# Kernel tuning notes

Measured on AMD Instinct MI355X. Metric: run time of the kernel, lower is better.

## Reference

```python
import jax, jax.numpy as jnp
import numpy as np

B, N, DH = 256, 32, 128      # batch, n_agents, per-agent hidden
E = 496                       # n_edges (fully connected over 32 agents)
DIM_IN = 2 * DH               # 256, MLP input (concat of two agent states)
DIM_HID = 256
A = 12                        # dim_act
R = 4                         # payoff_rank
DIM_OUT = 2 * R * A           # 96


def setup_inputs() -> dict:
    key = jax.random.key(0)
    ks = jax.random.split(key, 7)
    hidden_states_n = jax.random.normal(ks[0], (B, N, DH), dtype=jnp.float32)
    edges_from = jax.random.randint(ks[1], (E,), 0, N, dtype=jnp.int32).astype(jnp.int64)
    edges_to = jax.random.randint(ks[2], (E,), 0, N, dtype=jnp.int32).astype(jnp.int64)
    # torch.nn.Linear params: W [out, in], b [out]
    W1 = jax.random.normal(ks[3], (DIM_HID, DIM_IN), dtype=jnp.float32) * (1.0 / np.sqrt(DIM_IN))
    b1 = jnp.zeros((DIM_HID,), dtype=jnp.float32)
    W2 = jax.random.normal(ks[4], (DIM_OUT, DIM_HID), dtype=jnp.float32) * (1.0 / np.sqrt(DIM_HID))
    b2 = jnp.zeros((DIM_OUT,), dtype=jnp.float32)
    return {"hidden_states_n": hidden_states_n, "W1": W1, "b1": b1, "W2": W2,
            "b2": b2, "edges_from": edges_from, "edges_to": edges_to}


def reference(hidden_states_n, W1, b1, W2, b2, edges_from, edges_to):
    hf = hidden_states_n[:, edges_from]                     # [B, E, DH]
    ht = hidden_states_n[:, edges_to]                       # [B, E, DH]
    # stack of (from||to, to||from): [2, B, E, 2*DH]
    inp = jnp.stack([jnp.concatenate([hf, ht], axis=-1),
                     jnp.concatenate([ht, hf], axis=-1)], axis=0)
    h = jax.nn.relu(inp @ W1.T + b1)                        # [2, B, E, DIM_HID]
    p = h @ W2.T + b2                                       # [2, B, E, 2*R*A]
    p = p.reshape(2, B, E, R, 2, A)
    # low-rank outer product per rank, summed over ranks: [2, B, E, A, A]
    payoffs = jnp.einsum('sberi,sberj->sbeij', p[..., 0, :], p[..., 1, :])
    # second copy is transposed, then mean over the two directions
    return 0.5 * (payoffs[0] + jnp.swapaxes(payoffs[1], -1, -2))  # [B, E, A, A]
```

## Files before the change

### kernel.cpp

```cpp
#include <hip/hip_runtime.h>

typedef unsigned int uint;
typedef unsigned short ushort_t;

typedef __attribute__((ext_vector_type(8))) short bf16x8;
typedef __attribute__((ext_vector_type(4))) float f32x4;

#define E_CNT 496

__device__ __forceinline__ ushort_t f32_to_bf16_rn(float x) {
    uint u = __float_as_uint(x);
    u = (u + 0x7fffu + ((u >> 16) & 1u)) >> 16;
    return (ushort_t)u;
}
__device__ __forceinline__ uint pack2_bf16(float lo, float hi) {
    return (uint)f32_to_bf16_rn(lo) | ((uint)f32_to_bf16_rn(hi) << 16);
}

__global__ __launch_bounds__(256) void prep_kernel(
    const int* __restrict__ sf, const int* __restrict__ st,
    const float* __restrict__ W1, const float* __restrict__ W2,
    int* __restrict__ ef, int* __restrict__ et,
    ushort_t* __restrict__ w1img, ushort_t* __restrict__ w2img) {
    const int tid = threadIdx.x;
    const int blk = blockIdx.x;
    if (blk < 32) {
        int gid = blk * 256 + tid;
        int half = gid >> 12;
        int rem = gid & 4095;
        int h = rem >> 4;
        int c = rem & 15;
        const float* src = W1 + h * 256 + half * 128 + c * 8;
        float4 v0 = *(const float4*)src;
        float4 v1 = *(const float4*)(src + 4);
        uint4 o;
        o.x = pack2_bf16(v0.x, v0.y);
        o.y = pack2_bf16(v0.z, v0.w);
        o.z = pack2_bf16(v1.x, v1.y);
        o.w = pack2_bf16(v1.z, v1.w);
        int dst = half * 32768 + h * 128 + ((c ^ (h & 7)) << 3);
        *(uint4*)(w1img + dst) = o;
    } else if (blk < 44) {
        int gid = (blk - 32) * 256 + tid;
        int n = gid >> 5;
        int c = gid & 31;
        const float* src = W2 + n * 256 + c * 8;
        float4 v0 = *(const float4*)src;
        float4 v1 = *(const float4*)(src + 4);
        uint4 o;
        o.x = pack2_bf16(v0.x, v0.y);
        o.y = pack2_bf16(v0.z, v0.w);
        o.z = pack2_bf16(v1.x, v1.y);
        o.w = pack2_bf16(v1.z, v1.w);
        *(uint4*)(w2img + n * 264 + c * 8) = o;
    } else {
        bool f64 = true, t64 = true;
        #pragma unroll
        for (int i = 0; i < 16; ++i) {
            if (sf[2 * i + 1] != 0) f64 = false;
            if (st[2 * i + 1] != 0) t64 = false;
        }
        for (int j = tid; j < E_CNT; j += 256) {
            ef[j] = f64 ? sf[2 * j] : sf[j];
            et[j] = t64 ? st[2 * j] : st[j];
        }
    }
}

__global__ __launch_bounds__(256) void x_kernel(
    const float* __restrict__ hidden, const ushort_t* __restrict__ w1img,
    const float* __restrict__ b1, ushort_t* __restrict__ Xout) {
    __shared__ __align__(16) ushort_t w1s[256 * 128];

    const int tid = threadIdx.x;
    const int half = blockIdx.x & 1;
    const int mblk = blockIdx.x >> 1;

    {
        const uint4* gsrc = (const uint4*)(w1img + half * 32768);
        uint4* ldst = (uint4*)w1s;
        #pragma unroll
        for (int j = 0; j < 16; ++j) ldst[tid + j * 256] = gsrc[tid + j * 256];
    }

    const int ln = tid & 63;
    const int waveId = tid >> 6;
    const int quad = ln >> 4;
    const int l16 = ln & 15;
    const int row0 = mblk * 64 + waveId * 16;

    union { uint u[4]; bf16x8 v; } af[4];
    const float* arow = hidden + (row0 + l16) * 128 + quad * 8;
    #pragma unroll
    for (int kk = 0; kk < 4; ++kk) {
        float4 v0 = *(const float4*)(arow + kk * 32);
        float4 v1 = *(const float4*)(arow + kk * 32 + 4);
        af[kk].u[0] = pack2_bf16(v0.x, v0.y);
        af[kk].u[1] = pack2_bf16(v0.z, v0.w);
        af[kk].u[2] = pack2_bf16(v1.x, v1.y);
        af[kk].u[3] = pack2_bf16(v1.z, v1.w);
    }
    __syncthreads();

    ushort_t* xbase = Xout + half * (8192 * 256);
    #pragma unroll
    for (int nt = 0; nt < 16; ++nt) {
        const int h = nt * 16 + l16;
        f32x4 acc = (f32x4){0.f, 0.f, 0.f, 0.f};
        #pragma unroll
        for (int kk = 0; kk < 4; ++kk) {
            const int c_log = kk * 4 + quad;
            bf16x8 bf = *(const bf16x8*)&w1s[h * 128 + ((c_log ^ (h & 7)) << 3)];
            acc = __builtin_amdgcn_mfma_f32_16x16x32_bf16(af[kk].v, bf, acc, 0, 0, 0);
        }
        const float bh = 0.5f * b1[h];
        #pragma unroll
        for (int r = 0; r < 4; ++r) {
            const int row = row0 + quad * 4 + r;
            xbase[row * 256 + h] = f32_to_bf16_rn(acc[r] + bh);
        }
    }
}

#define PAIR_STRIDE 100
#define R_OFF 800
#define WAVE_PF 1600

__global__ __launch_bounds__(512, 4) void gemm_payoff_kernel(
    const ushort_t* __restrict__ X1, const ushort_t* __restrict__ X2,
    const int* __restrict__ ef, const int* __restrict__ et,
    const ushort_t* __restrict__ w2img, const float* __restrict__ b2,
    float* __restrict__ out) {

    __shared__ __align__(16) unsigned char smem[51200];
    ushort_t* w2s = (ushort_t*)smem;
    float* pf = (float*)smem;

    const int tid = threadIdx.x;

    {
        const uint4* src = (const uint4*)w2img;
        uint4* dst = (uint4*)smem;
        #pragma unroll
        for (int j = 0; j < 7; ++j) {
            int idx = tid + j * 512;
            if (idx < 3168) dst[idx] = src[idx];
        }
    }

    const int ln = tid & 63;
    const int waveId = tid >> 6;
    const int quad = ln >> 4;
    const int l16 = ln & 15;
    const int pl = l16 & 7;
    const int s = l16 >> 3;

    const int pairBase = blockIdx.x * 128 + waveId * 16;
    const ushort_t* px1[2];
    const ushort_t* px2[2];
    #pragma unroll
    for (int mt = 0; mt < 2; ++mt) {
        int pair = pairBase + mt * 8 + pl;
        int b = pair / E_CNT;
        int e = pair - b * E_CNT;
        int f = ef[e];
        int t = et[e];
        int n1 = s ? t : f;
        int n2 = s ? f : t;
        px1[mt] = X1 + ((b * 32 + n1) * 256 + quad * 8);
        px2[mt] = X2 + ((b * 32 + n2) * 256 + quad * 8);
    }

    float b2v[6];
    #pragma unroll
    for (int tt = 0; tt < 6; ++tt) b2v[tt] = b2[tt * 16 + l16];

    f32x4 acc[2][6];
    #pragma unroll
    for (int mt = 0; mt < 2; ++mt)
        #pragma unroll
        for (int tt = 0; tt < 6; ++tt) acc[mt][tt] = (f32x4){0.f, 0.f, 0.f, 0.f};

    __syncthreads();

    #pragma unroll
    for (int kk = 0; kk < 8; ++kk) {
        union { uint u[4]; bf16x8 v; } af[2];
        #pragma unroll
        for (int mt = 0; mt < 2; ++mt) {
            uint4 a1 = *(const uint4*)(px1[mt] + kk * 32);
            uint4 a2 = *(const uint4*)(px2[mt] + kk * 32);
            uint ua[4] = {a1.x, a1.y, a1.z, a1.w};
            uint ub[4] = {a2.x, a2.y, a2.z, a2.w};
            #pragma unroll
            for (int w = 0; w < 4; ++w) {
                float lo = __uint_as_float(ua[w] << 16) + __uint_as_float(ub[w] << 16);
                float hi = __uint_as_float(ua[w] & 0xffff0000u) + __uint_as_float(ub[w] & 0xffff0000u);
                lo = fmaxf(lo, 0.f);
                hi = fmaxf(hi, 0.f);
                af[mt].u[w] = (__float_as_uint(lo) >> 16) | (__float_as_uint(hi) & 0xffff0000u);
            }
        }
        #pragma unroll
        for (int tt = 0; tt < 6; ++tt) {
            bf16x8 bf = *(const bf16x8*)&w2s[(tt * 16 + l16) * 264 + kk * 32 + quad * 8];
            acc[0][tt] = __builtin_amdgcn_mfma_f32_16x16x32_bf16(af[0].v, bf, acc[0][tt], 0, 0, 0);
            acc[1][tt] = __builtin_amdgcn_mfma_f32_16x16x32_bf16(af[1].v, bf, acc[1][tt], 0, 0, 0);
        }
    }

    float* wbase = pf + waveId * WAVE_PF;
    #pragma unroll
    for (int mt = 0; mt < 2; ++mt) {
        __syncthreads();

        #pragma unroll
        for (int tt = 0; tt < 6; ++tt) {
            const int n = tt * 16 + l16;
            const int rr = n / 24;
            const int rem = n - rr * 24;
            const int c01 = (rem >= 12) ? 1 : 0;
            const int a = rem - c01 * 12;
            #pragma unroll
            for (int r = 0; r < 4; ++r) {
                const int row = quad * 4 + r;
                const int s_ = row >> 3;
                const int pl_ = row & 7;
                const int k8 = (s_ ? 4 : 0) + rr;
                const int toL = (c01 == s_) ? 1 : 0;
                wbase[(toL ? 0 : R_OFF) + pl_ * PAIR_STRIDE + a * 8 + k8] = acc[mt][tt][r] + b2v[tt];
            }
        }
        __syncthreads();

        #pragma unroll
        for (int it = 0; it < 2; ++it) {
            int task = it * 64 + ln;
            if (task < 96) {
                int pp = task / 12;
                int i = task - pp * 12;
                const float* Lp = wbase + pp * PAIR_STRIDE + i * 8;
                float4 l0 = *(const float4*)&Lp[0];
                float4 l1 = *(const float4*)&Lp[4];
                float od[12];
                #pragma unroll
                for (int jj = 0; jj < 12; ++jj) {
                    const float* Rp = wbase + R_OFF + pp * PAIR_STRIDE + jj * 8;
                    float4 r0 = *(const float4*)&Rp[0];
                    float4 r1 = *(const float4*)&Rp[4];
                    float d = l0.x * r0.x + l0.y * r0.y + l0.z * r0.z + l0.w * r0.w
                            + l1.x * r1.x + l1.y * r1.y + l1.z * r1.z + l1.w * r1.w;
                    od[jj] = 0.5f * d;
                }
                int outBase = (pairBase + mt * 8 + pp) * 144 + i * 12;
                *(float4*)&out[outBase + 0] = make_float4(od[0], od[1], od[2], od[3]);
                *(float4*)&out[outBase + 4] = make_float4(od[4], od[5], od[6], od[7]);
                *(float4*)&out[outBase + 8] = make_float4(od[8], od[9], od[10], od[11]);
            }
        }
    }
}

extern "C" void kernel_launch(void* const* d_in, const int* in_sizes, int n_in,
                              void* d_out, int out_size, void* d_ws, size_t ws_size,
                              hipStream_t stream) {
    const float* hidden = (const float*)d_in[0];
    const float* W1 = (const float*)d_in[1];
    const float* b1 = (const float*)d_in[2];
    const float* W2 = (const float*)d_in[3];
    const float* b2 = (const float*)d_in[4];
    const int* e_f = (const int*)d_in[5];
    const int* e_t = (const int*)d_in[6];
    float* out = (float*)d_out;

    char* ws = (char*)d_ws;
    int* ef = (int*)ws;
    int* et = (int*)(ws + 4096);
    ushort_t* w1img = (ushort_t*)(ws + 8192);
    ushort_t* w2img = (ushort_t*)(ws + 139264);
    ushort_t* X = (ushort_t*)(ws + 190464);

    prep_kernel<<<45, 256, 0, stream>>>(e_f, e_t, W1, W2, ef, et, w1img, w2img);
    x_kernel<<<256, 256, 0, stream>>>(hidden, w1img, b1, X);
    gemm_payoff_kernel<<<992, 512, 0, stream>>>(X, X + 8192 * 256, ef, et, w2img, b2, out);
}
```

Measured before the change: 146.9 us.

## Prefetch gathered rows, swizzle block order, and drop W1 LDS staging

The payoff GEMM now issues the gathered X1/X2 row loads in two register-double-buffered chunks, so global loads overlap the MFMA work instead of being issued just before each k-step. Block indices are remapped with an (bx&7)*124 + bx>>3 pattern to change how pairs are spread across XCDs. The per-iteration __syncthreads are removed from the epilogue, since each wave uses its own LDS region. In x_kernel, the 64KB LDS copy of W1 is dropped and each lane reads unswizzled W1 directly from global memory, which saves LDS setup and the barrier but depends on cache hits for the repeated weight reads.

New measurement: 147.8 us. No clear change (+0.6%).

```diff
diff --git a/kernel.cpp b/kernel.cpp
--- a/kernel.cpp
+++ b/kernel.cpp
@@ -38,8 +38,7 @@
         o.y = pack2_bf16(v0.z, v0.w);
         o.z = pack2_bf16(v1.x, v1.y);
         o.w = pack2_bf16(v1.z, v1.w);
-        int dst = half * 32768 + h * 128 + ((c ^ (h & 7)) << 3);
-        *(uint4*)(w1img + dst) = o;
+        *(uint4*)(w1img + half * 32768 + h * 128 + c * 8) = o;
     } else if (blk < 44) {
         int gid = (blk - 32) * 256 + tid;
         int n = gid >> 5;
@@ -70,18 +69,9 @@
 __global__ __launch_bounds__(256) void x_kernel(
     const float* __restrict__ hidden, const ushort_t* __restrict__ w1img,
     const float* __restrict__ b1, ushort_t* __restrict__ Xout) {
-    __shared__ __align__(16) ushort_t w1s[256 * 128];
-
     const int tid = threadIdx.x;
     const int half = blockIdx.x & 1;
     const int mblk = blockIdx.x >> 1;
-
-    {
-        const uint4* gsrc = (const uint4*)(w1img + half * 32768);
-        uint4* ldst = (uint4*)w1s;
-        #pragma unroll
-        for (int j = 0; j < 16; ++j) ldst[tid + j * 256] = gsrc[tid + j * 256];
-    }
 
     const int ln = tid & 63;
     const int waveId = tid >> 6;
@@ -100,19 +90,22 @@
         af[kk].u[2] = pack2_bf16(v1.x, v1.y);
         af[kk].u[3] = pack2_bf16(v1.z, v1.w);
     }
-    __syncthreads();
-
+
+    const ushort_t* wb = w1img + half * 32768;
     ushort_t* xbase = Xout + half * (8192 * 256);
-    #pragma unroll
+    #pragma unroll 4
     for (int nt = 0; nt < 16; ++nt) {
         const int h = nt * 16 + l16;
+        const ushort_t* wrow = wb + h * 128 + quad * 8;
+        bf16x8 bf0 = *(const bf16x8*)(wrow + 0 * 32);
+        bf16x8 bf1 = *(const bf16x8*)(wrow + 1 * 32);
+        bf16x8 bf2 = *(const bf16x8*)(wrow + 2 * 32);
+        bf16x8 bf3 = *(const bf16x8*)(wrow + 3 * 32);
         f32x4 acc = (f32x4){0.f, 0.f, 0.f, 0.f};
-        #pragma unroll
-        for (int kk = 0; kk < 4; ++kk) {
-            const int c_log = kk * 4 + quad;
-            bf16x8 bf = *(const bf16x8*)&w1s[h * 128 + ((c_log ^ (h & 7)) << 3)];
-            acc = __builtin_amdgcn_mfma_f32_16x16x32_bf16(af[kk].v, bf, acc, 0, 0, 0);
-        }
+        acc = __builtin_amdgcn_mfma_f32_16x16x32_bf16(af[0].v, bf0, acc, 0, 0, 0);
+        acc = __builtin_amdgcn_mfma_f32_16x16x32_bf16(af[1].v, bf1, acc, 0, 0, 0);
+        acc = __builtin_amdgcn_mfma_f32_16x16x32_bf16(af[2].v, bf2, acc, 0, 0, 0);
+        acc = __builtin_amdgcn_mfma_f32_16x16x32_bf16(af[3].v, bf3, acc, 0, 0, 0);
         const float bh = 0.5f * b1[h];
         #pragma unroll
         for (int r = 0; r < 4; ++r) {
@@ -155,7 +148,10 @@
     const int pl = l16 & 7;
     const int s = l16 >> 3;
 
-    const int pairBase = blockIdx.x * 128 + waveId * 16;
+    const int bx = blockIdx.x;
+    const int lb = (bx & 7) * 124 + (bx >> 3);
+
+    const int pairBase = lb * 128 + waveId * 16;
     const ushort_t* px1[2];
     const ushort_t* px2[2];
     #pragma unroll
@@ -171,49 +167,69 @@
         px2[mt] = X2 + ((b * 32 + n2) * 256 + quad * 8);
     }
 
+    f32x4 acc[2][6];
+    #pragma unroll
+    for (int mt = 0; mt < 2; ++mt)
+        #pragma unroll
+        for (int tt = 0; tt < 6; ++tt) acc[mt][tt] = (f32x4){0.f, 0.f, 0.f, 0.f};
+
+    uint4 GA1[2][2], GA2[2][2], GB1[2][2], GB2[2][2];
+
+    auto loadC = [&](uint4 G1[2][2], uint4 G2[2][2], int koff) {
+        #pragma unroll
+        for (int mt = 0; mt < 2; ++mt)
+            #pragma unroll
+            for (int k2 = 0; k2 < 2; ++k2) {
+                G1[mt][k2] = *(const uint4*)(px1[mt] + (koff + k2) * 32);
+                G2[mt][k2] = *(const uint4*)(px2[mt] + (koff + k2) * 32);
+            }
+    };
+    auto computeC = [&](uint4 G1[2][2], uint4 G2[2][2], int koff) {
+        #pragma unroll
+        for (int k2 = 0; k2 < 2; ++k2) {
+            const int kk = koff + k2;
+            union { uint u[4]; bf16x8 v; } af[2];
+            #pragma unroll
+            for (int mt = 0; mt < 2; ++mt) {
+                uint ua[4] = {G1[mt][k2].x, G1[mt][k2].y, G1[mt][k2].z, G1[mt][k2].w};
+                uint ub[4] = {G2[mt][k2].x, G2[mt][k2].y, G2[mt][k2].z, G2[mt][k2].w};
+                #pragma unroll
+                for (int w = 0; w < 4; ++w) {
+                    float lo = __uint_as_float(ua[w] << 16) + __uint_as_float(ub[w] << 16);
+                    float hi = __uint_as_float(ua[w] & 0xffff0000u) + __uint_as_float(ub[w] & 0xffff0000u);
+                    lo = fmaxf(lo, 0.f);
+                    hi = fmaxf(hi, 0.f);
+                    af[mt].u[w] = (__float_as_uint(lo) >> 16) | (__float_as_uint(hi) & 0xffff0000u);
+                }
+            }
+            #pragma unroll
+            for (int tt = 0; tt < 6; ++tt) {
+                bf16x8 bf = *(const bf16x8*)&w2s[(tt * 16 + l16) * 264 + kk * 32 + quad * 8];
+                acc[0][tt] = __builtin_amdgcn_mfma_f32_16x16x32_bf16(af[0].v, bf, acc[0][tt], 0, 0, 0);
+                acc[1][tt] = __builtin_amdgcn_mfma_f32_16x16x32_bf16(af[1].v, bf, acc[1][tt], 0, 0, 0);
+            }
+        }
+    };
+
+    loadC(GA1, GA2, 0);
+    loadC(GB1, GB2, 2);
+    __syncthreads();
+    computeC(GA1, GA2, 0);
+    loadC(GA1, GA2, 4);
+    computeC(GB1, GB2, 2);
+    loadC(GB1, GB2, 6);
+    computeC(GA1, GA2, 4);
+    computeC(GB1, GB2, 6);
+
     float b2v[6];
     #pragma unroll
     for (int tt = 0; tt < 6; ++tt) b2v[tt] = b2[tt * 16 + l16];
 
-    f32x4 acc[2][6];
-    #pragma unroll
-    for (int mt = 0; mt < 2; ++mt)
-        #pragma unroll
-        for (int tt = 0; tt < 6; ++tt) acc[mt][tt] = (f32x4){0.f, 0.f, 0.f, 0.f};
-
     __syncthreads();
 
-    #pragma unroll
-    for (int kk = 0; kk < 8; ++kk) {
-        union { uint u[4]; bf16x8 v; } af[2];
-        #pragma unroll
-        for (int mt = 0; mt < 2; ++mt) {
-            uint4 a1 = *(const uint4*)(px1[mt] + kk * 32);
-            uint4 a2 = *(const uint4*)(px2[mt] + kk * 32);
-            uint ua[4] = {a1.x, a1.y, a1.z, a1.w};
-            uint ub[4] = {a2.x, a2.y, a2.z, a2.w};
-            #pragma unroll
-            for (int w = 0; w < 4; ++w) {
-                float lo = __uint_as_float(ua[w] << 16) + __uint_as_float(ub[w] << 16);
-                float hi = __uint_as_float(ua[w] & 0xffff0000u) + __uint_as_float(ub[w] & 0xffff0000u);
-                lo = fmaxf(lo, 0.f);
-                hi = fmaxf(hi, 0.f);
-                af[mt].u[w] = (__float_as_uint(lo) >> 16) | (__float_as_uint(hi) & 0xffff0000u);
-            }
-        }
-        #pragma unroll
-        for (int tt = 0; tt < 6; ++tt) {
-            bf16x8 bf = *(const bf16x8*)&w2s[(tt * 16 + l16) * 264 + kk * 32 + quad * 8];
-            acc[0][tt] = __builtin_amdgcn_mfma_f32_16x16x32_bf16(af[0].v, bf, acc[0][tt], 0, 0, 0);
-            acc[1][tt] = __builtin_amdgcn_mfma_f32_16x16x32_bf16(af[1].v, bf, acc[1][tt], 0, 0, 0);
-        }
-    }
-
     float* wbase = pf + waveId * WAVE_PF;
     #pragma unroll
     for (int mt = 0; mt < 2; ++mt) {
-        __syncthreads();
-
         #pragma unroll
         for (int tt = 0; tt < 6; ++tt) {
             const int n = tt * 16 + l16;
@@ -231,7 +247,6 @@
                 wbase[(toL ? 0 : R_OFF) + pl_ * PAIR_STRIDE + a * 8 + k8] = acc[mt][tt][r] + b2v[tt];
             }
         }
-        __syncthreads();
 
         #pragma unroll
         for (int it = 0; it < 2; ++it) {
```

## Fold weight and edge prep into consumer kernels, prefetch gathered rows, trim syncs

Applied to the files above, without the earlier changes.

Drops the separate prep kernel. x_kernel now converts W1 to bf16 straight into its swizzled LDS layout, and every gemm_payoff block converts W2 into LDS and decodes the int64/int32 edge indices itself. This removes one launch and its dependency bubble, at the cost of redundant W2 conversion and extra global reads in each of the 992 blocks. The gemm kernel also double-buffers the gathered X rows in registers, remaps block indices to interleave batches, and keeps only one barrier in the epilogue because each wave's scratch region is private. In x_kernel the bias loads are hoisted and the output loop is only partly unrolled.

Measured after the change: 140.3 us. -4.5%, faster.

```diff
diff --git a/kernel.cpp b/kernel.cpp
--- a/kernel.cpp
+++ b/kernel.cpp
@@ -17,58 +17,8 @@
     return (uint)f32_to_bf16_rn(lo) | ((uint)f32_to_bf16_rn(hi) << 16);
 }
 
-__global__ __launch_bounds__(256) void prep_kernel(
-    const int* __restrict__ sf, const int* __restrict__ st,
-    const float* __restrict__ W1, const float* __restrict__ W2,
-    int* __restrict__ ef, int* __restrict__ et,
-    ushort_t* __restrict__ w1img, ushort_t* __restrict__ w2img) {
-    const int tid = threadIdx.x;
-    const int blk = blockIdx.x;
-    if (blk < 32) {
-        int gid = blk * 256 + tid;
-        int half = gid >> 12;
-        int rem = gid & 4095;
-        int h = rem >> 4;
-        int c = rem & 15;
-        const float* src = W1 + h * 256 + half * 128 + c * 8;
-        float4 v0 = *(const float4*)src;
-        float4 v1 = *(const float4*)(src + 4);
-        uint4 o;
-        o.x = pack2_bf16(v0.x, v0.y);
-        o.y = pack2_bf16(v0.z, v0.w);
-        o.z = pack2_bf16(v1.x, v1.y);
-        o.w = pack2_bf16(v1.z, v1.w);
-        int dst = half * 32768 + h * 128 + ((c ^ (h & 7)) << 3);
-        *(uint4*)(w1img + dst) = o;
-    } else if (blk < 44) {
-        int gid = (blk - 32) * 256 + tid;
-        int n = gid >> 5;
-        int c = gid & 31;
-        const float* src = W2 + n * 256 + c * 8;
-        float4 v0 = *(const float4*)src;
-        float4 v1 = *(const float4*)(src + 4);
-        uint4 o;
-        o.x = pack2_bf16(v0.x, v0.y);
-        o.y = pack2_bf16(v0.z, v0.w);
-        o.z = pack2_bf16(v1.x, v1.y);
-        o.w = pack2_bf16(v1.z, v1.w);
-        *(uint4*)(w2img + n * 264 + c * 8) = o;
-    } else {
-        bool f64 = true, t64 = true;
-        #pragma unroll
-        for (int i = 0; i < 16; ++i) {
-            if (sf[2 * i + 1] != 0) f64 = false;
-            if (st[2 * i + 1] != 0) t64 = false;
-        }
-        for (int j = tid; j < E_CNT; j += 256) {
-            ef[j] = f64 ? sf[2 * j] : sf[j];
-            et[j] = t64 ? st[2 * j] : st[j];
-        }
-    }
-}
-
 __global__ __launch_bounds__(256) void x_kernel(
-    const float* __restrict__ hidden, const ushort_t* __restrict__ w1img,
+    const float* __restrict__ hidden, const float* __restrict__ W1,
     const float* __restrict__ b1, ushort_t* __restrict__ Xout) {
     __shared__ __align__(16) ushort_t w1s[256 * 128];
 
@@ -77,10 +27,21 @@
     const int mblk = blockIdx.x >> 1;
 
     {
-        const uint4* gsrc = (const uint4*)(w1img + half * 32768);
-        uint4* ldst = (uint4*)w1s;
-        #pragma unroll
-        for (int j = 0; j < 16; ++j) ldst[tid + j * 256] = gsrc[tid + j * 256];
+        const int c = tid & 15;
+        const int h0 = tid >> 4;
+        #pragma unroll
+        for (int it = 0; it < 16; ++it) {
+            const int h = it * 16 + h0;
+            const float* src = W1 + h * 256 + half * 128 + c * 8;
+            float4 v0 = *(const float4*)src;
+            float4 v1 = *(const float4*)(src + 4);
+            uint4 o;
+            o.x = pack2_bf16(v0.x, v0.y);
+            o.y = pack2_bf16(v0.z, v0.w);
+            o.z = pack2_bf16(v1.x, v1.y);
+            o.w = pack2_bf16(v1.z, v1.w);
+            *(uint4*)&w1s[h * 128 + ((c ^ (h & 7)) << 3)] = o;
+        }
     }
 
     const int ln = tid & 63;
@@ -100,10 +61,14 @@
         af[kk].u[2] = pack2_bf16(v1.x, v1.y);
         af[kk].u[3] = pack2_bf16(v1.z, v1.w);
     }
+    float bh[16];
+    #pragma unroll
+    for (int nt = 0; nt < 16; ++nt) bh[nt] = 0.5f * b1[nt * 16 + l16];
+
     __syncthreads();
 
     ushort_t* xbase = Xout + half * (8192 * 256);
-    #pragma unroll
+    #pragma unroll 4
     for (int nt = 0; nt < 16; ++nt) {
         const int h = nt * 16 + l16;
         f32x4 acc = (f32x4){0.f, 0.f, 0.f, 0.f};
@@ -113,11 +78,10 @@
             bf16x8 bf = *(const bf16x8*)&w1s[h * 128 + ((c_log ^ (h & 7)) << 3)];
             acc = __builtin_amdgcn_mfma_f32_16x16x32_bf16(af[kk].v, bf, acc, 0, 0, 0);
         }
-        const float bh = 0.5f * b1[h];
         #pragma unroll
         for (int r = 0; r < 4; ++r) {
             const int row = row0 + quad * 4 + r;
-            xbase[row * 256 + h] = f32_to_bf16_rn(acc[r] + bh);
+            xbase[row * 256 + h] = f32_to_bf16_rn(acc[r] + bh[nt]);
         }
     }
 }
@@ -128,8 +92,8 @@
 
 __global__ __launch_bounds__(512, 4) void gemm_payoff_kernel(
     const ushort_t* __restrict__ X1, const ushort_t* __restrict__ X2,
-    const int* __restrict__ ef, const int* __restrict__ et,
-    const ushort_t* __restrict__ w2img, const float* __restrict__ b2,
+    const int* __restrict__ e_f, const int* __restrict__ e_t,
+    const float* __restrict__ W2, const float* __restrict__ b2,
     float* __restrict__ out) {
 
     __shared__ __align__(16) unsigned char smem[51200];
@@ -138,14 +102,16 @@
 
     const int tid = threadIdx.x;
 
-    {
-        const uint4* src = (const uint4*)w2img;
-        uint4* dst = (uint4*)smem;
-        #pragma unroll
-        for (int j = 0; j < 7; ++j) {
-            int idx = tid + j * 512;
-            if (idx < 3168) dst[idx] = src[idx];
-        }
+    #pragma unroll
+    for (int j = 0; j < 12; ++j) {
+        int idx4 = tid + j * 512;
+        int n = idx4 >> 6;
+        int k = (idx4 & 63) << 2;
+        float4 v = *(const float4*)&W2[n * 256 + k];
+        uint2 o;
+        o.x = pack2_bf16(v.x, v.y);
+        o.y = pack2_bf16(v.z, v.w);
+        *(uint2*)&w2s[n * 264 + k] = o;
     }
 
     const int ln = tid & 63;
@@ -155,7 +121,17 @@
     const int pl = l16 & 7;
     const int s = l16 >> 3;
 
-    const int pairBase = blockIdx.x * 128 + waveId * 16;
+    const int bx = blockIdx.x;
+    const int lb = (bx & 7) * 124 + (bx >> 3);
+
+    bool f64 = true, t64 = true;
+    #pragma unroll
+    for (int i = 0; i < 16; ++i) {
+        if (e_f[2 * i + 1] != 0) f64 = false;
+        if (e_t[2 * i + 1] != 0) t64 = false;
+    }
+
+    const int pairBase = lb * 128 + waveId * 16;
     const ushort_t* px1[2];
     const ushort_t* px2[2];
     #pragma unroll
@@ -163,35 +139,40 @@
         int pair = pairBase + mt * 8 + pl;
         int b = pair / E_CNT;
         int e = pair - b * E_CNT;
-        int f = ef[e];
-        int t = et[e];
+        int f = f64 ? e_f[2 * e] : e_f[e];
+        int t = t64 ? e_t[2 * e] : e_t[e];
         int n1 = s ? t : f;
         int n2 = s ? f : t;
         px1[mt] = X1 + ((b * 32 + n1) * 256 + quad * 8);
         px2[mt] = X2 + ((b * 32 + n2) * 256 + quad * 8);
     }
 
-    float b2v[6];
-    #pragma unroll
-    for (int tt = 0; tt < 6; ++tt) b2v[tt] = b2[tt * 16 + l16];
-
     f32x4 acc[2][6];
     #pragma unroll
     for (int mt = 0; mt < 2; ++mt)
         #pragma unroll
         for (int tt = 0; tt < 6; ++tt) acc[mt][tt] = (f32x4){0.f, 0.f, 0.f, 0.f};
 
+    uint4 G1[2][2], G2[2][2];
+
+    #pragma unroll
+    for (int mt = 0; mt < 2; ++mt) {
+        G1[0][mt] = *(const uint4*)(px1[mt] + 0 * 32);
+        G2[0][mt] = *(const uint4*)(px2[mt] + 0 * 32);
+        G1[1][mt] = *(const uint4*)(px1[mt] + 1 * 32);
+        G2[1][mt] = *(const uint4*)(px2[mt] + 1 * 32);
+    }
+
     __syncthreads();
 
     #pragma unroll
     for (int kk = 0; kk < 8; ++kk) {
+        const int buf = kk & 1;
         union { uint u[4]; bf16x8 v; } af[2];
         #pragma unroll
         for (int mt = 0; mt < 2; ++mt) {
-            uint4 a1 = *(const uint4*)(px1[mt] + kk * 32);
-            uint4 a2 = *(const uint4*)(px2[mt] + kk * 32);
-            uint ua[4] = {a1.x, a1.y, a1.z, a1.w};
-            uint ub[4] = {a2.x, a2.y, a2.z, a2.w};
+            uint ua[4] = {G1[buf][mt].x, G1[buf][mt].y, G1[buf][mt].z, G1[buf][mt].w};
+            uint ub[4] = {G2[buf][mt].x, G2[buf][mt].y, G2[buf][mt].z, G2[buf][mt].w};
             #pragma unroll
             for (int w = 0; w < 4; ++w) {
                 float lo = __uint_as_float(ua[w] << 16) + __uint_as_float(ub[w] << 16);
@@ -201,6 +182,13 @@
                 af[mt].u[w] = (__float_as_uint(lo) >> 16) | (__float_as_uint(hi) & 0xffff0000u);
             }
         }
+        if (kk < 6) {
+            #pragma unroll
+            for (int mt = 0; mt < 2; ++mt) {
+                G1[buf][mt] = *(const uint4*)(px1[mt] + (kk + 2) * 32);
+                G2[buf][mt] = *(const uint4*)(px2[mt] + (kk + 2) * 32);
+            }
+        }
         #pragma unroll
         for (int tt = 0; tt < 6; ++tt) {
             bf16x8 bf = *(const bf16x8*)&w2s[(tt * 16 + l16) * 264 + kk * 32 + quad * 8];
@@ -209,11 +197,15 @@
         }
     }
 
+    float b2v[6];
+    #pragma unroll
+    for (int tt = 0; tt < 6; ++tt) b2v[tt] = b2[tt * 16 + l16];
+
+    __syncthreads();
+
     float* wbase = pf + waveId * WAVE_PF;
     #pragma unroll
     for (int mt = 0; mt < 2; ++mt) {
-        __syncthreads();
-
         #pragma unroll
         for (int tt = 0; tt < 6; ++tt) {
             const int n = tt * 16 + l16;
@@ -231,7 +223,6 @@
                 wbase[(toL ? 0 : R_OFF) + pl_ * PAIR_STRIDE + a * 8 + k8] = acc[mt][tt][r] + b2v[tt];
             }
         }
-        __syncthreads();
 
         #pragma unroll
         for (int it = 0; it < 2; ++it) {
@@ -274,13 +265,8 @@
     float* out = (float*)d_out;
 
     char* ws = (char*)d_ws;
-    int* ef = (int*)ws;
-    int* et = (int*)(ws + 4096);
-    ushort_t* w1img = (ushort_t*)(ws + 8192);
-    ushort_t* w2img = (ushort_t*)(ws + 139264);
-    ushort_t* X = (ushort_t*)(ws + 190464);
-
-    prep_kernel<<<45, 256, 0, stream>>>(e_f, e_t, W1, W2, ef, et, w1img, w2img);
-    x_kernel<<<256, 256, 0, stream>>>(hidden, w1img, b1, X);
-    gemm_payoff_kernel<<<992, 512, 0, stream>>>(X, X + 8192 * 256, ef, et, w2img, b2, out);
-}
+    ushort_t* X = (ushort_t*)ws;
+
+    x_kernel<<<256, 256, 0, stream>>>(hidden, W1, b1, X);
+    gemm_payoff_kernel<<<992, 512, 0, stream>>>(X, X + 8192 * 256, e_f, e_t, W2, b2, out);
+}
```
